# Kernel optimization log

Hardware: AMD Instinct MI355X
Metric: run time of the kernel (lower is better)

The kernel has to match this reference:

```python
import jax, jax.numpy as jnp
import numpy as np

N = 50000          # nodes
E = 1_600_000      # edges (avg degree 32)
D = 128            # in_channels
H = 4              # heads
C = 32             # out_channels per head (H*C == D for residual add)
NEG_SLOPE = 0.2
STEPS = 3


def setup_inputs() -> dict:
    key = jax.random.key(0)
    k1, k2, k3, k4, k5 = jax.random.split(key, 5)
    x = jax.random.normal(k1, (N, D), jnp.float32)
    edge_index = jax.random.randint(k2, (2, E), 0, N)  # row0=src, row1=dst
    W = jax.random.normal(k3, (D, H * C), jnp.float32) * (1.0 / np.sqrt(D))
    a_src = jax.random.normal(k4, (H, C), jnp.float32) * 0.1
    a_dst = jax.random.normal(k5, (H, C), jnp.float32) * 0.1
    return {"x": x, "edge_index": edge_index, "W": W,
            "a_src": a_src, "a_dst": a_dst, "steps": STEPS}


def _attn_conv(x, edge_index, W, a_src, a_dst):
    """One GAT-style attention conv. Returns (out [N,H*C], attn [E,H], logits [E,H])."""
    src, dst = edge_index[0], edge_index[1]
    h = (x @ W).reshape(N, H, C)                      # [N,H,C]
    alpha_src = jnp.einsum('nhc,hc->nh', h, a_src)    # [N,H]
    alpha_dst = jnp.einsum('nhc,hc->nh', h, a_dst)    # [N,H]
    logits = jax.nn.leaky_relu(alpha_src[src] + alpha_dst[dst], NEG_SLOPE)  # [E,H]
    # softmax over incoming edges of each destination node (segment softmax)
    m = jax.ops.segment_max(logits, dst, num_segments=N)      # [N,H]
    m = jnp.where(jnp.isfinite(m), m, 0.0)                    # nodes w/o in-edges
    e = jnp.exp(logits - m[dst])                              # [E,H]
    denom = jax.ops.segment_sum(e, dst, num_segments=N)       # [N,H]
    attn = e / (denom[dst] + 1e-16)                           # [E,H]
    msg = h[src] * attn[..., None]                            # [E,H,C]
    out = jax.ops.segment_sum(msg, dst, num_segments=N)       # [N,H,C]
    return out.reshape(N, H * C), attn, logits


def reference(x, edge_index, W, a_src, a_dst, steps):
    x_s, attn_s, rel_s = [], [], []
    for _ in range(steps):  # fixed small step count, matches the torch Python loop
        x_prime, attn_t, rel_t = _attn_conv(x, edge_index, W, a_src, a_dst)
        x = x + x_prime
        x_s.append(x)
        attn_s.append(attn_t)
        rel_s.append(rel_t)
    return jnp.stack(x_s, 0), jnp.stack(attn_s, 0), jnp.stack(rel_s, 0)
```

## Files before the change

### kernel.cpp

```cpp
#include <hip/hip_runtime.h>
#include <hip/hip_bf16.h>
#include <math.h>

#define NN 50000
#define EE 1600000
#define DD 128
#define HH 4
#define NSTEP 3
#define NEG 0.2f
#define BM 32
#define NPB 8
#define CAPN 128
#define NPART 4
#define SEGC 32

typedef unsigned short ushort8v __attribute__((ext_vector_type(8)));
typedef float float4v __attribute__((ext_vector_type(4)));

__device__ __forceinline__ float leaky(float v) { return v >= 0.0f ? v : NEG * v; }

__device__ __forceinline__ unsigned short bfu(float f) {
    __hip_bfloat16 b = __float2bfloat16(f);
    return *reinterpret_cast<unsigned short*>(&b);
}
__device__ __forceinline__ float ubf(unsigned short u) {
    return __uint_as_float(((unsigned int)u) << 16);
}

__global__ __launch_bounds__(256) void gemm_k2(const float* __restrict__ X,
                                               const float* __restrict__ W,
                                               const float* __restrict__ a_src,
                                               const float* __restrict__ a_dst,
                                               unsigned short* __restrict__ Hb,
                                               float* __restrict__ as_,
                                               float4* __restrict__ nd) {
    __shared__ float xs[BM][132];
    const int tid  = threadIdx.x;
    const int tcol = tid & 31;
    const int trow = tid >> 5;
    const int row0 = blockIdx.x * BM;

    #pragma unroll
    for (int i = 0; i < 4; ++i) {
        const int l  = tid + 256 * i;
        const int r  = l >> 5;
        const int c4 = l & 31;
        float4 v = {0.f, 0.f, 0.f, 0.f};
        if (row0 + r < NN) v = ((const float4*)(X + (size_t)(row0 + r) * DD))[c4];
        *(float4*)&xs[r][c4 * 4] = v;
    }
    __syncthreads();

    const float4* __restrict__ W4 = (const float4*)W;
    float4 acc0 = {0,0,0,0}, acc1 = {0,0,0,0}, acc2 = {0,0,0,0}, acc3 = {0,0,0,0};

    for (int k = 0; k < DD; k += 4) {
        float4 wv0 = W4[(k + 0) * 32 + tcol];
        float4 wv1 = W4[(k + 1) * 32 + tcol];
        float4 wv2 = W4[(k + 2) * 32 + tcol];
        float4 wv3 = W4[(k + 3) * 32 + tcol];
        float4 xv0 = *(const float4*)&xs[4 * trow + 0][k];
        float4 xv1 = *(const float4*)&xs[4 * trow + 1][k];
        float4 xv2 = *(const float4*)&xs[4 * trow + 2][k];
        float4 xv3 = *(const float4*)&xs[4 * trow + 3][k];
        #define GSTEP(ACC, XV) \
            ACC.x += XV.x * wv0.x; ACC.y += XV.x * wv0.y; ACC.z += XV.x * wv0.z; ACC.w += XV.x * wv0.w; \
            ACC.x += XV.y * wv1.x; ACC.y += XV.y * wv1.y; ACC.z += XV.y * wv1.z; ACC.w += XV.y * wv1.w; \
            ACC.x += XV.z * wv2.x; ACC.y += XV.z * wv2.y; ACC.z += XV.z * wv2.z; ACC.w += XV.z * wv2.w; \
            ACC.x += XV.w * wv3.x; ACC.y += XV.w * wv3.y; ACC.z += XV.w * wv3.z; ACC.w += XV.w * wv3.w;
        GSTEP(acc0, xv0) GSTEP(acc1, xv1) GSTEP(acc2, xv2) GSTEP(acc3, xv3)
        #undef GSTEP
    }

    const float4 asv = ((const float4*)a_src)[tcol];
    const float4 adv = ((const float4*)a_dst)[tcol];
    float ps0 = acc0.x*asv.x + acc0.y*asv.y + acc0.z*asv.z + acc0.w*asv.w;
    float ps1 = acc1.x*asv.x + acc1.y*asv.y + acc1.z*asv.z + acc1.w*asv.w;
    float ps2 = acc2.x*asv.x + acc2.y*asv.y + acc2.z*asv.z + acc2.w*asv.w;
    float ps3 = acc3.x*asv.x + acc3.y*asv.y + acc3.z*asv.z + acc3.w*asv.w;
    float pd0 = acc0.x*adv.x + acc0.y*adv.y + acc0.z*adv.z + acc0.w*adv.w;
    float pd1 = acc1.x*adv.x + acc1.y*adv.y + acc1.z*adv.z + acc1.w*adv.w;
    float pd2 = acc2.x*adv.x + acc2.y*adv.y + acc2.z*adv.z + acc2.w*adv.w;
    float pd3 = acc3.x*adv.x + acc3.y*adv.y + acc3.z*adv.z + acc3.w*adv.w;
    #pragma unroll
    for (int off = 1; off < 8; off <<= 1) {
        ps0 += __shfl_xor(ps0, off); ps1 += __shfl_xor(ps1, off);
        ps2 += __shfl_xor(ps2, off); ps3 += __shfl_xor(ps3, off);
        pd0 += __shfl_xor(pd0, off); pd1 += __shfl_xor(pd1, off);
        pd2 += __shfl_xor(pd2, off); pd3 += __shfl_xor(pd3, off);
    }

    #pragma unroll
    for (int i = 0; i < 4; ++i) {
        const int row = row0 + 4 * trow + i;
        if (row >= NN) break;
        const float4 a = (i == 0) ? acc0 : (i == 1) ? acc1 : (i == 2) ? acc2 : acc3;
        ushort4 p;
        p.x = bfu(a.x); p.y = bfu(a.y); p.z = bfu(a.z); p.w = bfu(a.w);
        *(ushort4*)&Hb[(size_t)row * DD + 4 * tcol] = p;
    }
    if ((tcol & 7) == 0) {
        const int head = tcol >> 3;
        #pragma unroll
        for (int i = 0; i < 4; ++i) {
            const int row = row0 + 4 * trow + i;
            if (row >= NN) break;
            const float ps = (i == 0) ? ps0 : (i == 1) ? ps1 : (i == 2) ? ps2 : ps3;
            const float pd = (i == 0) ? pd0 : (i == 1) ? pd1 : (i == 2) ? pd2 : pd3;
            as_[(size_t)row * HH + head] = ps;
            ((float*)(nd + (size_t)row * 3))[head] = pd;
        }
    }
}

__global__ __launch_bounds__(256) void zero_k(int* __restrict__ p, int n) {
    const int i = blockIdx.x * 256 + threadIdx.x;
    if (i < n) p[i] = 0;
}

__global__ __launch_bounds__(256) void scat_k(const int* __restrict__ ei,
                                              int* __restrict__ cursor,
                                              unsigned short* __restrict__ csr) {
    const int e = blockIdx.x * 256 + threadIdx.x;
    if (e >= EE) return;
    const int s = ei[e], d = ei[EE + e];
    const int c = d * NPART + (e & (NPART - 1));
    const int pos = atomicAdd(&cursor[c], 1);
    if (pos < SEGC) csr[(size_t)c * SEGC + pos] = (unsigned short)s;
}

__global__ __launch_bounds__(256) void node_k3(const int* __restrict__ cursor,
                                               const unsigned short* __restrict__ csr,
                                               const float* __restrict__ as_,
                                               float4* __restrict__ nd,
                                               const unsigned short* __restrict__ Hb,
                                               const float* __restrict__ xprev,
                                               float* __restrict__ xout) {
    __shared__ int    src_l[NPB][CAPN];
    __shared__ float4 exp_l[NPB][CAPN];

    const int tid  = threadIdx.x;
    const int nl   = tid >> 5;
    const int lane = tid & 31;
    const int n    = blockIdx.x * NPB + nl;

    const int cbase = n * NPART;
    int degs[NPART];
    int deg = 0;
    #pragma unroll
    for (int p = 0; p < NPART; ++p) {
        int dp = cursor[cbase + p];
        if (dp > SEGC) dp = SEGC;
        degs[p] = dp;
        deg += dp;
    }

    if (deg == 0) {
        ((float4*)(xout + (size_t)n * DD))[lane] = ((const float4*)(xprev + (size_t)n * DD))[lane];
        return;
    }

    const float4 adv = nd[(size_t)n * 3];

    float4 mx = {-INFINITY, -INFINITY, -INFINITY, -INFINITY};
    int off = 0;
    #pragma unroll
    for (int p = 0; p < NPART; ++p) {
        if (lane < degs[p]) {
            const int s = (int)csr[(size_t)(cbase + p) * SEGC + lane];
            const float4 av = *(const float4*)(as_ + (size_t)s * HH);
            float4 l;
            l.x = leaky(av.x + adv.x); l.y = leaky(av.y + adv.y);
            l.z = leaky(av.z + adv.z); l.w = leaky(av.w + adv.w);
            src_l[nl][off + lane] = s; exp_l[nl][off + lane] = l;
            mx.x = fmaxf(mx.x, l.x); mx.y = fmaxf(mx.y, l.y);
            mx.z = fmaxf(mx.z, l.z); mx.w = fmaxf(mx.w, l.w);
        }
        off += degs[p];
    }
    #pragma unroll
    for (int o = 1; o < 32; o <<= 1) {
        mx.x = fmaxf(mx.x, __shfl_xor(mx.x, o));
        mx.y = fmaxf(mx.y, __shfl_xor(mx.y, o));
        mx.z = fmaxf(mx.z, __shfl_xor(mx.z, o));
        mx.w = fmaxf(mx.w, __shfl_xor(mx.w, o));
    }

    float4 ds = {0.f, 0.f, 0.f, 0.f};
    for (int j = lane; j < deg; j += 32) {
        const float4 l = exp_l[nl][j];
        float4 e4;
        e4.x = expf(l.x - mx.x); e4.y = expf(l.y - mx.y);
        e4.z = expf(l.z - mx.z); e4.w = expf(l.w - mx.w);
        exp_l[nl][j] = e4;
        ds.x += e4.x; ds.y += e4.y; ds.z += e4.z; ds.w += e4.w;
    }
    #pragma unroll
    for (int o = 1; o < 32; o <<= 1) {
        ds.x += __shfl_xor(ds.x, o); ds.y += __shfl_xor(ds.y, o);
        ds.z += __shfl_xor(ds.z, o); ds.w += __shfl_xor(ds.w, o);
    }
    float4 inv;
    inv.x = 1.0f / (ds.x + 1e-16f); inv.y = 1.0f / (ds.y + 1e-16f);
    inv.z = 1.0f / (ds.z + 1e-16f); inv.w = 1.0f / (ds.w + 1e-16f);

    if (lane == 0) {
        nd[(size_t)n * 3 + 1] = mx;
        nd[(size_t)n * 3 + 2] = inv;
    }

    const int esel = lane >> 4;
    const int sub  = lane & 15;
    const int hsel = sub >> 2;
    const float invh = (hsel == 0) ? inv.x : (hsel == 1) ? inv.y : (hsel == 2) ? inv.z : inv.w;
    float4 aclo = {0.f, 0.f, 0.f, 0.f};
    float4 achi = {0.f, 0.f, 0.f, 0.f};
    int j0 = 0;
    #pragma unroll 2
    for (; j0 + 2 <= deg; j0 += 2) {
        const int j = j0 + esel;
        const int s = src_l[nl][j];
        const float a = ((const float*)&exp_l[nl][j])[hsel] * invh;
        const ushort8v hv = *(const ushort8v*)&Hb[(size_t)s * DD + 8 * sub];
        aclo.x += ubf(hv[0]) * a; aclo.y += ubf(hv[1]) * a;
        aclo.z += ubf(hv[2]) * a; aclo.w += ubf(hv[3]) * a;
        achi.x += ubf(hv[4]) * a; achi.y += ubf(hv[5]) * a;
        achi.z += ubf(hv[6]) * a; achi.w += ubf(hv[7]) * a;
    }
    if (j0 < deg && esel == 0) {
        const int j = j0;
        const int s = src_l[nl][j];
        const float a = ((const float*)&exp_l[nl][j])[hsel] * invh;
        const ushort8v hv = *(const ushort8v*)&Hb[(size_t)s * DD + 8 * sub];
        aclo.x += ubf(hv[0]) * a; aclo.y += ubf(hv[1]) * a;
        aclo.z += ubf(hv[2]) * a; aclo.w += ubf(hv[3]) * a;
        achi.x += ubf(hv[4]) * a; achi.y += ubf(hv[5]) * a;
        achi.z += ubf(hv[6]) * a; achi.w += ubf(hv[7]) * a;
    }
    aclo.x += __shfl_xor(aclo.x, 16); aclo.y += __shfl_xor(aclo.y, 16);
    aclo.z += __shfl_xor(aclo.z, 16); aclo.w += __shfl_xor(aclo.w, 16);
    achi.x += __shfl_xor(achi.x, 16); achi.y += __shfl_xor(achi.y, 16);
    achi.z += __shfl_xor(achi.z, 16); achi.w += __shfl_xor(achi.w, 16);
    const float4 mine = (esel == 0) ? aclo : achi;
    const int fidx = 2 * sub + esel;
    const float4 xv = ((const float4*)(xprev + (size_t)n * DD))[fidx];
    float4 o;
    o.x = xv.x + mine.x; o.y = xv.y + mine.y; o.z = xv.z + mine.z; o.w = xv.w + mine.w;
    ((float4*)(xout + (size_t)n * DD))[fidx] = o;
}

__global__ __launch_bounds__(256) void edgeattn3_k(const int* __restrict__ ei,
                                                   const float* __restrict__ as3,
                                                   const float4* __restrict__ nd3,
                                                   float* __restrict__ rel_out,
                                                   float* __restrict__ attn_out) {
    const int e = blockIdx.x * 256 + threadIdx.x;
    if (e >= EE) return;
    const int st = blockIdx.y;
    const int s = __builtin_nontemporal_load(ei + e);
    const int d = __builtin_nontemporal_load(ei + EE + e);
    const float4 av = *(const float4*)(as3 + ((size_t)st * NN + s) * HH);
    const float4* ndp = nd3 + ((size_t)st * NN + d) * 3;
    const float4 dv = ndp[0];
    const float4 mm = ndp[1];
    const float4 iv = ndp[2];
    float4v l;
    l.x = leaky(av.x + dv.x); l.y = leaky(av.y + dv.y);
    l.z = leaky(av.z + dv.z); l.w = leaky(av.w + dv.w);
    __builtin_nontemporal_store(l, (float4v*)(rel_out + ((size_t)st * EE + e) * HH));
    float4v a;
    a.x = expf(l.x - mm.x) * iv.x; a.y = expf(l.y - mm.y) * iv.y;
    a.z = expf(l.z - mm.z) * iv.z; a.w = expf(l.w - mm.w) * iv.w;
    __builtin_nontemporal_store(a, (float4v*)(attn_out + ((size_t)st * EE + e) * HH));
}

extern "C" void kernel_launch(void* const* d_in, const int* in_sizes, int n_in,
                              void* d_out, int out_size, void* d_ws, size_t ws_size,
                              hipStream_t stream) {
    const float* x     = (const float*)d_in[0];
    const int*   ei    = (const int*)d_in[1];
    const float* W     = (const float*)d_in[2];
    const float* a_src = (const float*)d_in[3];
    const float* a_dst = (const float*)d_in[4];

    float* xs_out   = (float*)d_out;
    float* attn_out = xs_out + (size_t)NSTEP * NN * DD;
    float* rel_out  = attn_out + (size_t)NSTEP * EE * HH;

    unsigned short* hb = (unsigned short*)d_ws;
    float*  as3   = (float*)(hb + (size_t)NN * DD);
    float4* nd3   = (float4*)(as3 + (size_t)NSTEP * NN * HH);
    int*    cursor = (int*)(nd3 + (size_t)NSTEP * NN * 3);
    unsigned short* csr = (unsigned short*)(cursor + (size_t)NN * NPART);

    zero_k<<<(NN * NPART + 255) / 256, 256, 0, stream>>>(cursor, NN * NPART);
    scat_k<<<(EE + 255) / 256, 256, 0, stream>>>(ei, cursor, csr);

    const float* xprev = x;
    for (int s = 0; s < NSTEP; ++s) {
        float* xs_s = xs_out + (size_t)s * NN * DD;
        float* as_  = as3 + (size_t)s * NN * HH;
        float4* nd  = nd3 + (size_t)s * NN * 3;

        gemm_k2<<<(NN + BM - 1) / BM, 256, 0, stream>>>(xprev, W, a_src, a_dst, hb, as_, nd);
        node_k3<<<NN / NPB, 256, 0, stream>>>(cursor, csr, as_, nd, hb, xprev, xs_s);
        xprev = xs_s;
    }
    dim3 eg((EE + 255) / 256, NSTEP);
    edgeattn3_k<<<eg, 256, 0, stream>>>(ei, as3, nd3, rel_out, attn_out);
}
```

Baseline: 507.0 us.

## Replace per-node atomic scatter with two-pass bucketed counting-sort CSR build

The edge-to-destination CSR construction moves from a global-atomic scatter into fixed 4x32 slots per node to a two-pass bucket sort. The first pass groups edges into 256-node buckets using shared-memory histograms; the second does a per-bucket counting sort to produce contiguous rows with a start offset and degree. The node kernel then reads one contiguous row per node instead of four partitioned segments. This cuts global atomic contention and the per-partition cap of 32, but adds an extra pass over the edge keys, and buckets are capped at 9216 edges.

```diff
diff --git a/kernel.cpp b/kernel.cpp
--- a/kernel.cpp
+++ b/kernel.cpp
@@ -11,8 +11,10 @@
 #define BM 32
 #define NPB 8
 #define CAPN 128
-#define NPART 4
-#define SEGC 32
+#define NBUCK 196
+#define BUCKCAP 9216
+#define P1CH 16384
+#define NB1 ((EE + P1CH - 1) / P1CH)
 
 typedef unsigned short ushort8v __attribute__((ext_vector_type(8)));
 typedef float float4v __attribute__((ext_vector_type(4)));
@@ -118,18 +120,75 @@
     if (i < n) p[i] = 0;
 }
 
-__global__ __launch_bounds__(256) void scat_k(const int* __restrict__ ei,
-                                              int* __restrict__ cursor,
-                                              unsigned short* __restrict__ csr) {
-    const int e = blockIdx.x * 256 + threadIdx.x;
-    if (e >= EE) return;
-    const int s = ei[e], d = ei[EE + e];
-    const int c = d * NPART + (e & (NPART - 1));
-    const int pos = atomicAdd(&cursor[c], 1);
-    if (pos < SEGC) csr[(size_t)c * SEGC + pos] = (unsigned short)s;
-}
-
-__global__ __launch_bounds__(256) void node_k3(const int* __restrict__ cursor,
+__global__ __launch_bounds__(256) void p1_k(const int* __restrict__ ei,
+                                            int* __restrict__ bcur,
+                                            unsigned int* __restrict__ bkeys) {
+    __shared__ int hist[NBUCK];
+    __shared__ int cur[NBUCK];
+    const int tid = threadIdx.x;
+    const int e0 = blockIdx.x * P1CH;
+    const int e1 = (e0 + P1CH < EE) ? e0 + P1CH : EE;
+
+    for (int i = tid; i < NBUCK; i += 256) hist[i] = 0;
+    __syncthreads();
+    for (int e = e0 + tid; e < e1; e += 256)
+        atomicAdd(&hist[ei[EE + e] >> 8], 1);
+    __syncthreads();
+    for (int i = tid; i < NBUCK; i += 256)
+        cur[i] = (hist[i] > 0) ? atomicAdd(&bcur[i], hist[i]) : 0;
+    __syncthreads();
+    for (int e = e0 + tid; e < e1; e += 256) {
+        const int s = ei[e];
+        const int d = ei[EE + e];
+        const int b = d >> 8;
+        const int pos = atomicAdd(&cur[b], 1);
+        if (pos < BUCKCAP)
+            bkeys[(size_t)b * BUCKCAP + pos] = ((unsigned int)d << 16) | (unsigned int)s;
+    }
+}
+
+__global__ __launch_bounds__(256) void p2_k(const int* __restrict__ bcur,
+                                            const unsigned int* __restrict__ bkeys,
+                                            int* __restrict__ row_start,
+                                            int* __restrict__ degA,
+                                            unsigned short* __restrict__ csr) {
+    __shared__ int hist[256];
+    __shared__ int offs[256];
+    __shared__ int cur[256];
+    const int b = blockIdx.x;
+    const int tid = threadIdx.x;
+    int ne = bcur[b]; if (ne > BUCKCAP) ne = BUCKCAP;
+    const unsigned int* keys = bkeys + (size_t)b * BUCKCAP;
+
+    hist[tid] = 0;
+    __syncthreads();
+    for (int i = tid; i < ne; i += 256)
+        atomicAdd(&hist[(keys[i] >> 16) & 255], 1);
+    __syncthreads();
+    const int v = hist[tid];
+    offs[tid] = v;
+    __syncthreads();
+    for (int o = 1; o < 256; o <<= 1) {
+        const int add = (tid >= o) ? offs[tid - o] : 0;
+        __syncthreads();
+        offs[tid] += add;
+        __syncthreads();
+    }
+    const int excl = offs[tid] - v;
+    const int n = (b << 8) + tid;
+    if (n < NN) { row_start[n] = b * BUCKCAP + excl; degA[n] = v; }
+    cur[tid] = excl;
+    __syncthreads();
+    for (int i = tid; i < ne; i += 256) {
+        const unsigned int k = keys[i];
+        const int local = (int)((k >> 16) & 255);
+        const int pos = atomicAdd(&cur[local], 1);
+        csr[(size_t)b * BUCKCAP + pos] = (unsigned short)(k & 0xFFFF);
+    }
+}
+
+__global__ __launch_bounds__(256) void node_k3(const int* __restrict__ row_start,
+                                               const int* __restrict__ degA,
                                                const unsigned short* __restrict__ csr,
                                                const float* __restrict__ as_,
                                                float4* __restrict__ nd,
@@ -144,16 +203,9 @@
     const int lane = tid & 31;
     const int n    = blockIdx.x * NPB + nl;
 
-    const int cbase = n * NPART;
-    int degs[NPART];
-    int deg = 0;
-    #pragma unroll
-    for (int p = 0; p < NPART; ++p) {
-        int dp = cursor[cbase + p];
-        if (dp > SEGC) dp = SEGC;
-        degs[p] = dp;
-        deg += dp;
-    }
+    int deg = degA[n];
+    if (deg > CAPN) deg = CAPN;
+    const int row0 = row_start[n];
 
     if (deg == 0) {
         ((float4*)(xout + (size_t)n * DD))[lane] = ((const float4*)(xprev + (size_t)n * DD))[lane];
@@ -163,20 +215,15 @@
     const float4 adv = nd[(size_t)n * 3];
 
     float4 mx = {-INFINITY, -INFINITY, -INFINITY, -INFINITY};
-    int off = 0;
-    #pragma unroll
-    for (int p = 0; p < NPART; ++p) {
-        if (lane < degs[p]) {
-            const int s = (int)csr[(size_t)(cbase + p) * SEGC + lane];
-            const float4 av = *(const float4*)(as_ + (size_t)s * HH);
-            float4 l;
-            l.x = leaky(av.x + adv.x); l.y = leaky(av.y + adv.y);
-            l.z = leaky(av.z + adv.z); l.w = leaky(av.w + adv.w);
-            src_l[nl][off + lane] = s; exp_l[nl][off + lane] = l;
-            mx.x = fmaxf(mx.x, l.x); mx.y = fmaxf(mx.y, l.y);
-            mx.z = fmaxf(mx.z, l.z); mx.w = fmaxf(mx.w, l.w);
-        }
-        off += degs[p];
+    for (int j = lane; j < deg; j += 32) {
+        const int s = (int)csr[(size_t)row0 + j];
+        const float4 av = *(const float4*)(as_ + (size_t)s * HH);
+        float4 l;
+        l.x = leaky(av.x + adv.x); l.y = leaky(av.y + adv.y);
+        l.z = leaky(av.z + adv.z); l.w = leaky(av.w + adv.w);
+        src_l[nl][j] = s; exp_l[nl][j] = l;
+        mx.x = fmaxf(mx.x, l.x); mx.y = fmaxf(mx.y, l.y);
+        mx.z = fmaxf(mx.z, l.z); mx.w = fmaxf(mx.w, l.w);
     }
     #pragma unroll
     for (int o = 1; o < 32; o <<= 1) {
@@ -290,11 +337,15 @@
     unsigned short* hb = (unsigned short*)d_ws;
     float*  as3   = (float*)(hb + (size_t)NN * DD);
     float4* nd3   = (float4*)(as3 + (size_t)NSTEP * NN * HH);
-    int*    cursor = (int*)(nd3 + (size_t)NSTEP * NN * 3);
-    unsigned short* csr = (unsigned short*)(cursor + (size_t)NN * NPART);
-
-    zero_k<<<(NN * NPART + 255) / 256, 256, 0, stream>>>(cursor, NN * NPART);
-    scat_k<<<(EE + 255) / 256, 256, 0, stream>>>(ei, cursor, csr);
+    int*    bcur  = (int*)(nd3 + (size_t)NSTEP * NN * 3);
+    unsigned int* bkeys = (unsigned int*)(bcur + NBUCK);
+    int*    rowst = (int*)(bkeys + (size_t)NBUCK * BUCKCAP);
+    int*    degA  = rowst + NN;
+    unsigned short* csr = (unsigned short*)(degA + NN);
+
+    zero_k<<<1, 256, 0, stream>>>(bcur, NBUCK);
+    p1_k<<<NB1, 256, 0, stream>>>(ei, bcur, bkeys);
+    p2_k<<<NBUCK, 256, 0, stream>>>(bcur, bkeys, rowst, degA, csr);
 
     const float* xprev = x;
     for (int s = 0; s < NSTEP; ++s) {
@@ -303,7 +354,7 @@
         float4* nd  = nd3 + (size_t)s * NN * 3;
 
         gemm_k2<<<(NN + BM - 1) / BM, 256, 0, stream>>>(xprev, W, a_src, a_dst, hb, as_, nd);
-        node_k3<<<NN / NPB, 256, 0, stream>>>(cursor, csr, as_, nd, hb, xprev, xs_s);
+        node_k3<<<NN / NPB, 256, 0, stream>>>(rowst, degA, csr, as_, nd, hb, xprev, xs_s);
         xprev = xs_s;
     }
     dim3 eg((EE + 255) / 256, NSTEP);
```

Measured after the change: 477.2 us (median of 2 runs). 5.9% less time.
